# Kernel tuning notes

Hardware: AMD Instinct MI355X
Metric: run time of the kernel (lower is better)

Reference implementation:

```python
import jax, jax.numpy as jnp
import numpy as np

B, M, H = 1024, 32, 2
D = 64
N_ENT = 500000
N_REL = 32


def setup_inputs() -> dict:
    key = jax.random.key(0)
    k1, k2, k3, k4 = jax.random.split(key, 4)
    edge_index = jax.random.randint(k1, (B, 2), 0, N_ENT, dtype=jnp.int64)
    # column 0: head entity ids, column 1: relation ids; keep both < N_REL so both are in-range
    ripple_sets = jax.random.randint(k2, (H, B, M, 2), 0, N_REL, dtype=jnp.int64)
    entity_emb = jax.random.normal(k3, (N_ENT, D), dtype=jnp.float32)
    relation_emb = jax.random.normal(k4, (N_REL, D * D), dtype=jnp.float32)
    # padding_idx=0 -> row 0 is zeros
    entity_emb = entity_emb.at[0].set(0.0)
    relation_emb = relation_emb.at[0].set(0.0)
    return {
        "edge_index": edge_index,
        "ripple_sets": ripple_sets,
        "entity_emb": entity_emb,
        "relation_emb": relation_emb,
    }


def reference(edge_index, ripple_sets, entity_emb, relation_emb):
    d = entity_emb.shape[1]
    item = entity_emb[edge_index[:, 1]]            # [B, d]
    u = jnp.zeros_like(item)                       # [B, d]
    for hop in range(ripple_sets.shape[0]):        # small fixed hop count
        rs = ripple_sets[hop]                      # [B, M, 2]
        R = relation_emb[rs[:, :, 1]].reshape(rs.shape[0], -1, d, d)  # [B, M, d, d]
        h = entity_emb[rs[:, :, 0]]                # [B, M, d]
        Rh = jnp.einsum('bmij,bmj->bmi', R, h)     # [B, M, d]
        vRh = jnp.einsum('bmi,bi->bm', Rh, item)   # [B, M]
        p = jax.nn.softmax(vRh, axis=1)            # [B, M]
        u = u + jnp.einsum('bm,bmd->bd', p, h)     # weighted sum of tails (t == h)
    return jnp.sum(u * item, axis=1, keepdims=True)  # [B, 1]
```

## Files before the change

kernel.cpp:

```cpp
#include <hip/hip_runtime.h>
#include <math.h>

#define BB   1024
#define MM   32
#define HH   2
#define DD   64
#define NREL 32
#define TBB  32

__global__ __launch_bounds__(256) void compute_q(
    const int* __restrict__ edge_index,
    const float* __restrict__ entity_emb,
    const float* __restrict__ relation_emb,
    float* __restrict__ qout)
{
    __shared__ float R_s[DD * DD];
    __shared__ float item_s[TBB * 68];

    const int r   = blockIdx.y;
    const int b0  = blockIdx.x * TBB;
    const int tid = threadIdx.x;

    const float4* Rg = (const float4*)(relation_emb + (size_t)r * DD * DD);
    #pragma unroll
    for (int k = 0; k < 4; ++k)
        ((float4*)R_s)[tid + 256 * k] = Rg[tid + 256 * k];

    #pragma unroll
    for (int k = 0; k < 2; ++k) {
        int idx = tid + 256 * k;
        int bl  = idx >> 4;
        int c4  = idx & 15;
        int ei  = edge_index[2 * (b0 + bl) + 1];
        ((float4*)(item_s + bl * 68))[c4] =
            *(const float4*)(entity_emb + (size_t)ei * DD + c4 * 4);
    }
    __syncthreads();

    const int j4  = (tid & 15) * 4;
    const int bl0 = tid >> 4;
    float4 acc0 = {0.f, 0.f, 0.f, 0.f};
    float4 acc1 = {0.f, 0.f, 0.f, 0.f};
    #pragma unroll 8
    for (int i = 0; i < DD; ++i) {
        const float4 rv = *(const float4*)(R_s + i * DD + j4);
        const float a0 = item_s[bl0 * 68 + i];
        const float a1 = item_s[(bl0 + 16) * 68 + i];
        acc0.x += a0 * rv.x; acc0.y += a0 * rv.y;
        acc0.z += a0 * rv.z; acc0.w += a0 * rv.w;
        acc1.x += a1 * rv.x; acc1.y += a1 * rv.y;
        acc1.z += a1 * rv.z; acc1.w += a1 * rv.w;
    }
    size_t q0 = ((size_t)(b0 + bl0) * NREL + r) * DD + j4;
    size_t q1 = ((size_t)(b0 + bl0 + 16) * NREL + r) * DD + j4;
    *(float4*)(qout + q0) = acc0;
    *(float4*)(qout + q1) = acc1;
}

#define HS 65

__global__ __launch_bounds__(256) void ripple_apply(
    const int* __restrict__ edge_index,
    const int* __restrict__ ripple_sets,
    const float* __restrict__ entity_emb,
    const float* __restrict__ qg,
    float* __restrict__ out)
{
    __shared__ float item_s[DD];
    __shared__ float h_s[HH * MM * HS];
    __shared__ float q_s[HH * MM * HS];
    __shared__ int   head_s[HH * MM];
    __shared__ int   rel_s[HH * MM];
    __shared__ float v_s[HH * MM];
    __shared__ float p_s[HH * MM];

    const int b   = blockIdx.x;
    const int tid = threadIdx.x;

    if (tid < DD) {
        int item_idx = edge_index[2 * b + 1];
        item_s[tid] = entity_emb[(size_t)item_idx * DD + tid];
    }
    if (tid < HH * MM) {
        int hop = tid >> 5, m = tid & 31;
        size_t base = ((size_t)(hop * BB + b) * MM + m) * 2;
        head_s[tid] = ripple_sets[base];
        rel_s[tid]  = ripple_sets[base + 1];
    }
    __syncthreads();

    #pragma unroll
    for (int k = 0; k < 4; ++k) {
        int idx = tid + 256 * k;
        int row = idx >> 4;
        int c4  = idx & 15;
        const float4 hv = *(const float4*)(entity_emb + (size_t)head_s[row] * DD + c4 * 4);
        float* hd = h_s + row * HS + c4 * 4;
        hd[0] = hv.x; hd[1] = hv.y; hd[2] = hv.z; hd[3] = hv.w;
        const float4 qv = *(const float4*)(qg + ((size_t)b * NREL + rel_s[row]) * DD + c4 * 4);
        float* qd = q_s + row * HS + c4 * 4;
        qd[0] = qv.x; qd[1] = qv.y; qd[2] = qv.z; qd[3] = qv.w;
    }
    __syncthreads();

    if (tid < HH * MM) {
        const float* qp = q_s + tid * HS;
        const float* hp = h_s + tid * HS;
        float acc = 0.f;
        #pragma unroll
        for (int j = 0; j < DD; ++j) acc += qp[j] * hp[j];
        v_s[tid] = acc;
    }
    __syncthreads();

    if (tid < HH) {
        const float* vv = v_s + tid * MM;
        float* pp = p_s + tid * MM;
        float mx = vv[0];
        for (int m = 1; m < MM; ++m) mx = fmaxf(mx, vv[m]);
        float s = 0.f;
        for (int m = 0; m < MM; ++m) { float e = expf(vv[m] - mx); pp[m] = e; s += e; }
        float inv = 1.f / s;
        for (int m = 0; m < MM; ++m) pp[m] *= inv;
    }
    __syncthreads();

    if (tid < DD) {
        float u = 0.f;
        #pragma unroll
        for (int t = 0; t < HH * MM; ++t) u += p_s[t] * h_s[t * HS + tid];
        float prod = u * item_s[tid];
        #pragma unroll
        for (int off = 32; off > 0; off >>= 1) prod += __shfl_down(prod, off, 64);
        if (tid == 0) out[b] = prod;
    }
}

extern "C" void kernel_launch(void* const* d_in, const int* in_sizes, int n_in,
                              void* d_out, int out_size, void* d_ws, size_t ws_size,
                              hipStream_t stream) {
    const int*   edge_index   = (const int*)d_in[0];
    const int*   ripple_sets  = (const int*)d_in[1];
    const float* entity_emb   = (const float*)d_in[2];
    const float* relation_emb = (const float*)d_in[3];
    float* out = (float*)d_out;
    float* qbuf = (float*)d_ws;
    (void)in_sizes; (void)n_in; (void)out_size; (void)ws_size;

    compute_q<<<dim3(BB / TBB, NREL), dim3(256), 0, stream>>>(
        edge_index, entity_emb, relation_emb, qbuf);
    ripple_apply<<<dim3(BB), dim3(256), 0, stream>>>(
        edge_index, ripple_sets, entity_emb, qbuf, out);
}
```

Baseline: 175.2 us.

## Parallelize ripple_apply dot products, softmax and weighted sum across all threads

Spreads the per-row q·h dot products and the p-weighted sum of h across all 256 threads, each handling a quarter of the work, with partial sums combined through shared memory. The serial two-thread softmax becomes a wavefront shuffle reduction over 32 lanes. Ripple-set indices are now loaded directly in the gather loop, which removes one sync and the index staging arrays. This trades extra shared memory and partial-sum syncs for shorter serial phases in the per-batch block.

```diff
diff --git a/kernel.cpp b/kernel.cpp
--- a/kernel.cpp
+++ b/kernel.cpp
@@ -69,10 +69,9 @@
     __shared__ float item_s[DD];
     __shared__ float h_s[HH * MM * HS];
     __shared__ float q_s[HH * MM * HS];
-    __shared__ int   head_s[HH * MM];
-    __shared__ int   rel_s[HH * MM];
-    __shared__ float v_s[HH * MM];
+    __shared__ float vp_s[4 * 64];
     __shared__ float p_s[HH * MM];
+    __shared__ float up_s[4 * 68];
 
     const int b   = blockIdx.x;
     const int tid = threadIdx.x;
@@ -81,54 +80,67 @@
         int item_idx = edge_index[2 * b + 1];
         item_s[tid] = entity_emb[(size_t)item_idx * DD + tid];
     }
-    if (tid < HH * MM) {
-        int hop = tid >> 5, m = tid & 31;
-        size_t base = ((size_t)(hop * BB + b) * MM + m) * 2;
-        head_s[tid] = ripple_sets[base];
-        rel_s[tid]  = ripple_sets[base + 1];
-    }
-    __syncthreads();
 
     #pragma unroll
     for (int k = 0; k < 4; ++k) {
         int idx = tid + 256 * k;
         int row = idx >> 4;
         int c4  = idx & 15;
-        const float4 hv = *(const float4*)(entity_emb + (size_t)head_s[row] * DD + c4 * 4);
+        int hop = row >> 5, m = row & 31;
+        size_t ibase = ((size_t)(hop * BB + b) * MM + m) * 2;
+        int head = ripple_sets[ibase];
+        int rel  = ripple_sets[ibase + 1];
+        const float4 hv = *(const float4*)(entity_emb + (size_t)head * DD + c4 * 4);
         float* hd = h_s + row * HS + c4 * 4;
         hd[0] = hv.x; hd[1] = hv.y; hd[2] = hv.z; hd[3] = hv.w;
-        const float4 qv = *(const float4*)(qg + ((size_t)b * NREL + rel_s[row]) * DD + c4 * 4);
+        const float4 qv = *(const float4*)(qg + ((size_t)b * NREL + rel) * DD + c4 * 4);
         float* qd = q_s + row * HS + c4 * 4;
         qd[0] = qv.x; qd[1] = qv.y; qd[2] = qv.z; qd[3] = qv.w;
     }
     __syncthreads();
 
-    if (tid < HH * MM) {
-        const float* qp = q_s + tid * HS;
-        const float* hp = h_s + tid * HS;
+    {
+        int t = tid & 63;
+        int q = tid >> 6;
+        const float* qp = q_s + t * HS + q * 16;
+        const float* hp = h_s + t * HS + q * 16;
         float acc = 0.f;
         #pragma unroll
-        for (int j = 0; j < DD; ++j) acc += qp[j] * hp[j];
-        v_s[tid] = acc;
+        for (int j = 0; j < 16; ++j) acc += qp[j] * hp[j];
+        vp_s[q * 64 + t] = acc;
     }
     __syncthreads();
 
-    if (tid < HH) {
-        const float* vv = v_s + tid * MM;
-        float* pp = p_s + tid * MM;
-        float mx = vv[0];
-        for (int m = 1; m < MM; ++m) mx = fmaxf(mx, vv[m]);
-        float s = 0.f;
-        for (int m = 0; m < MM; ++m) { float e = expf(vv[m] - mx); pp[m] = e; s += e; }
-        float inv = 1.f / s;
-        for (int m = 0; m < MM; ++m) pp[m] *= inv;
+    if (tid < HH * MM) {
+        float v = vp_s[tid] + vp_s[64 + tid] + vp_s[128 + tid] + vp_s[192 + tid];
+        float mx = v;
+        #pragma unroll
+        for (int off = 16; off > 0; off >>= 1)
+            mx = fmaxf(mx, __shfl_xor(mx, off, 64));
+        float e = expf(v - mx);
+        float s = e;
+        #pragma unroll
+        for (int off = 16; off > 0; off >>= 1)
+            s += __shfl_xor(s, off, 64);
+        p_s[tid] = e / s;
+    }
+    __syncthreads();
+
+    {
+        int d    = tid & 63;
+        int part = tid >> 6;
+        float u = 0.f;
+        #pragma unroll
+        for (int tt = 0; tt < 16; ++tt) {
+            int t = part * 16 + tt;
+            u += p_s[t] * h_s[t * HS + d];
+        }
+        up_s[part * 68 + d] = u;
     }
     __syncthreads();
 
     if (tid < DD) {
-        float u = 0.f;
-        #pragma unroll
-        for (int t = 0; t < HH * MM; ++t) u += p_s[t] * h_s[t * HS + tid];
+        float u = up_s[tid] + up_s[68 + tid] + up_s[136 + tid] + up_s[204 + tid];
         float prod = u * item_s[tid];
         #pragma unroll
         for (int off = 32; off > 0; off >>= 1) prod += __shfl_down(prod, off, 64);
```

Result: faster. 170.8 us (median of 2 runs) (-2.5%).
